# Performance work log

Hardware: AMD Instinct MI355X
Metric: run time of the kernel (lower is better)

Reference implementation:

```python
import jax, jax.numpy as jnp
import numpy as np

STRIDE = 32
NUM_CLASSES = 20
CONF_THRESH = 0.01
NMS_THRESH = 0.5
INPUT_H, INPUT_W = 1024, 1024
EPS = 1e-28


def make_grid(h, w):
    hs, ws = h // STRIDE, w // STRIDE
    gy, gx = jnp.meshgrid(jnp.arange(hs), jnp.arange(ws), indexing='ij')
    # [1, hs*ws, 2] (x, y) cell coordinates
    return jnp.stack([gx, gy], axis=-1).reshape(1, hs * ws, 2).astype(jnp.float32)


def decode_boxes(txtytwth, grid):
    # txtytwth: [B, N, 4] -> [xmin, ymin, xmax, ymax] in pixels
    cxy = (jax.nn.sigmoid(txtytwth[..., :2]) + grid) * STRIDE
    wh = jnp.exp(txtytwth[..., 2:])
    return jnp.concatenate([cxy - wh * 0.5, cxy + wh * 0.5], axis=-1)


def pairwise_iou(boxes):
    # boxes: [N, 4]; faithful to source: area without +1, w/h clamped to 1e-28
    x1, y1, x2, y2 = boxes[:, 0], boxes[:, 1], boxes[:, 2], boxes[:, 3]
    areas = (x2 - x1) * (y2 - y1)
    xx1 = jnp.maximum(x1[:, None], x1[None, :])
    yy1 = jnp.maximum(y1[:, None], y1[None, :])
    xx2 = jnp.minimum(x2[:, None], x2[None, :])
    yy2 = jnp.minimum(y2[:, None], y2[None, :])
    w = jnp.maximum(EPS, xx2 - xx1)
    h = jnp.maximum(EPS, yy2 - yy1)
    inter = w * h
    return inter / (areas[:, None] + areas[None, :] - inter)


def nms_single(boxes, scores, valid):
    # greedy NMS, fixed-shape: returns keep mask [N] in original order
    n = boxes.shape[0]
    order = jnp.argsort(-scores)
    b = boxes[order]
    v = valid[order]
    iou = pairwise_iou(b)  # [N, N]
    idx = jnp.arange(n)

    def body(i, keep):
        sup = keep[i] & (iou[i] > NMS_THRESH) & (idx > i)
        return keep & jnp.logical_not(sup)

    keep_sorted = jax.lax.fori_loop(0, n, body, v)
    return jnp.zeros(n, dtype=bool).at[order].set(keep_sorted)


def setup_inputs() -> dict:
    key = jax.random.key(0)
    k1, k2, k3 = jax.random.split(key, 3)
    feat = jax.random.normal(k1, (64, 512, 32, 32), dtype=jnp.float32)
    w_pred = jax.random.normal(k2, (25, 512), dtype=jnp.float32) * 0.05
    b_pred = jax.random.normal(k3, (25,), dtype=jnp.float32) * 0.05
    return {"feat": feat, "w_pred": w_pred, "b_pred": b_pred}


def reference(feat, w_pred, b_pred):
    B, C, hs, ws = feat.shape
    N = hs * ws
    # 1x1 conv head: [B, 25, hs, ws] -> [B, N, 25]
    pred = jnp.einsum('bchw,oc->bhwo', feat, w_pred) + b_pred
    pred = pred.reshape(B, N, 1 + NUM_CLASSES + 4)

    conf = jax.nn.sigmoid(pred[..., :1])                      # [B, N, 1]
    cls = jax.nn.softmax(pred[..., 1:1 + NUM_CLASSES], -1)    # [B, N, 20]
    boxes = decode_boxes(pred[..., 1 + NUM_CLASSES:], make_grid(INPUT_H, INPUT_W))
    scale = jnp.array([INPUT_W, INPUT_H, INPUT_W, INPUT_H], jnp.float32)
    boxes = jnp.clip(boxes / scale, 0.0, 1.0)                 # [B, N, 4] in [0,1]

    scores_all = conf * cls                                   # [B, N, 20]
    cls_inds = jnp.argmax(scores_all, axis=-1)                # [B, N]
    scores = jnp.max(scores_all, axis=-1)                     # [B, N]
    valid = scores > CONF_THRESH

    # class-aware NMS via per-class coordinate offset (boxes in [0,1])
    off_boxes = boxes + cls_inds[..., None].astype(jnp.float32) * 2.0
    keep = jax.vmap(nms_single)(off_boxes, scores, valid)     # [B, N] bool
    return boxes, scores, cls_inds.astype(jnp.int32), keep
```

## Files before the change

### kernel.cpp

```cpp
#include <hip/hip_runtime.h>
#include <hip/hip_bf16.h>

typedef unsigned long long u64;
typedef unsigned int u32;
typedef __attribute__((ext_vector_type(4))) double f64x4;

#define NB   64
#define NPOS 1024
#define NOUT 25
#define NCLS 20
#define BIGCAP 256
#define ECAP   2048
#define TINY_TH (30.0f / 1024.0f)

#define OFF_CNT   0
#define OFF_BIGL  512
#define OFF_EDGL  66048

__device__ __forceinline__ void epilogue(const double* __restrict__ acc,
                                         const float* __restrict__ bias,
                                         int b, int n,
                                         float* __restrict__ boxes_out,
                                         float* __restrict__ scores_out,
                                         float* __restrict__ cls_out,
                                         int* __restrict__ bigcnt,
                                         int* __restrict__ biglist)
{
    double p[NOUT];
#pragma unroll
    for (int o = 0; o < NOUT; ++o) p[o] = acc[o] + (double)bias[o];

    double conf = 1.0 / (1.0 + exp(-p[0]));
    double m = p[1]; int ci = 0;
#pragma unroll
    for (int i = 2; i <= NCLS; ++i) {
        if (p[i] > m) { m = p[i]; ci = i - 1; }
    }
    double ssum = 0.0;
#pragma unroll
    for (int i = 0; i < NCLS; ++i) ssum += exp(p[1 + i] - m);
    double best = conf / ssum;

    int gx = n & 31, gy = n >> 5;
    double sx = 1.0 / (1.0 + exp(-p[21]));
    double sy = 1.0 / (1.0 + exp(-p[22]));
    double cx = (sx + (double)gx) * 32.0;
    double cy = (sy + (double)gy) * 32.0;
    double bw = exp(p[23]), bh = exp(p[24]);
    double x1 = (cx - bw * 0.5) * (1.0 / 1024.0);
    double y1 = (cy - bh * 0.5) * (1.0 / 1024.0);
    double x2 = (cx + bw * 0.5) * (1.0 / 1024.0);
    double y2 = (cy + bh * 0.5) * (1.0 / 1024.0);
    x1 = fmin(fmax(x1, 0.0), 1.0); y1 = fmin(fmax(y1, 0.0), 1.0);
    x2 = fmin(fmax(x2, 0.0), 1.0); y2 = fmin(fmax(y2, 0.0), 1.0);

    float fx1 = (float)x1, fy1 = (float)y1, fx2 = (float)x2, fy2 = (float)y2;
    int gi = b * NPOS + n;
    ((float4*)boxes_out)[gi] = make_float4(fx1, fy1, fx2, fy2);
    scores_out[gi] = (float)best;
    cls_out[gi]    = (float)ci;

    if (!((fx2 - fx1 < TINY_TH) && (fy2 - fy1 < TINY_TH))) {
        int s = atomicAdd(&bigcnt[b], 1);
        if (s < BIGCAP) biglist[b * BIGCAP + s] = n;
    }
}

__device__ __forceinline__ float4 loadB(const float* __restrict__ w, int c, int bo4)
{
    float4 r = make_float4(0.f, 0.f, 0.f, 0.f);
    int o = bo4 * 4;
    if (o + 0 < NOUT) r.x = w[(o + 0) * 512 + c];
    if (o + 1 < NOUT) r.y = w[(o + 1) * 512 + c];
    if (o + 2 < NOUT) r.z = w[(o + 2) * 512 + c];
    if (o + 3 < NOUT) r.w = w[(o + 3) * 512 + c];
    return r;
}

__global__ __launch_bounds__(256, 6) void k_main(const float* __restrict__ feat,
                                                 const float* __restrict__ w,
                                                 const float* __restrict__ bias,
                                                 float* __restrict__ boxes_out,
                                                 float* __restrict__ scores_out,
                                                 float* __restrict__ cls_out,
                                                 int* __restrict__ bigcnt,
                                                 int* __restrict__ biglist)
{
    __shared__ __align__(16) char smem[24576];
    float* AbF = (float*)smem;
    float* BbF = (float*)(smem + 16384);
    double (*pd)[33] = (double(*)[33])smem;

    const int b   = blockIdx.y;
    const int tid = threadIdx.x;
    const int l   = tid & 63;
    const int wv  = tid >> 6;
    const int pg  = wv >> 1;
    const int oh  = wv & 1;
    const int n0  = blockIdx.x * 64;

    double ca = ((l >> 4) == 0) ? (double)(l & 15) : 0.0;
    double cb = ((l >> 4) == 0) ? 1.0 : 0.0;
    f64x4 cd = {0.0, 0.0, 0.0, 0.0};
    cd = __builtin_amdgcn_mfma_f64_16x16x4f64(ca, cb, cd, 0, 0, 0);
    int rmap[4];
#pragma unroll
    for (int v = 0; v < 4; ++v) {
        int r = (int)(cd[v] + 0.5);
        rmap[v] = (r < 0) ? 0 : (r > 15 ? 15 : r);
    }

    const float* __restrict__ featb = feat + (size_t)b * 512 * NPOS + n0;
    const int bch = tid >> 3, bo4 = tid & 7;

#define A_SRC(C0, IT) (((const float4*)(featb + (size_t)((C0) + wv*8 + (IT)*4 + (l>>4)) * NPOS)) + (l & 15))
#define A_DST(BUF, IT) ((float4*)(AbF + (BUF)*2048 + (wv*8 + (IT)*4) * 64 + l*4))
#define B_DST(BUF) ((float4*)(BbF + (BUF)*1024 + bch*32 + bo4*4))

    f64x4 acc0 = {0.0, 0.0, 0.0, 0.0};
    f64x4 acc1 = {0.0, 0.0, 0.0, 0.0};

    float4 ra0 = *A_SRC(0, 0), ra1 = *A_SRC(0, 1);
    float4 rb  = loadB(w, bch, bo4);
    *A_DST(0, 0) = ra0;  *A_DST(0, 1) = ra1;
    *B_DST(0) = rb;
    __syncthreads();

#pragma unroll 1
    for (int t = 0; t < 16; ++t) {
        const int buf = t & 1;
        const bool more = (t + 1) < 16;
        const int c1 = (t + 1) * 32;
        if (more) {
            ra0 = *A_SRC(c1, 0);  ra1 = *A_SRC(c1, 1);
            rb  = loadB(w, c1 + bch, bo4);
        }
#pragma unroll
        for (int s = 0; s < 8; ++s) {
            const int rowA = buf*2048 + (4*s + (l >> 4)) * 64 + pg * 32 + (l & 15);
            const int rowB = buf*1024 + (4*s + (l >> 4)) * 32 + oh * 16 + (l & 15);
            double av0 = (double)AbF[rowA];
            double av1 = (double)AbF[rowA + 16];
            double bv  = (double)BbF[rowB];
            acc0 = __builtin_amdgcn_mfma_f64_16x16x4f64(av0, bv, acc0, 0, 0, 0);
            acc1 = __builtin_amdgcn_mfma_f64_16x16x4f64(av1, bv, acc1, 0, 0, 0);
        }
        if (more) {
            *A_DST(buf ^ 1, 0) = ra0;  *A_DST(buf ^ 1, 1) = ra1;
            *B_DST(buf ^ 1) = rb;
        }
        __syncthreads();
    }
#undef A_SRC
#undef A_DST
#undef B_DST

#pragma unroll
    for (int v = 0; v < 4; ++v) {
        int r0 = pg * 32 + rmap[v];
        pd[r0][oh * 16 + (l & 15)]      = acc0[v];
        pd[r0 + 16][oh * 16 + (l & 15)] = acc1[v];
    }
    __syncthreads();

    if (tid < 64) {
        double acc[NOUT];
#pragma unroll
        for (int o = 0; o < NOUT; ++o) acc[o] = pd[tid][o];
        int n = n0 + tid;
        epilogue(acc, bias, b, n, boxes_out, scores_out, cls_out, bigcnt, biglist);
    }
}

__device__ __forceinline__ void pair_check(int b, int p, int i,
                                           float4 bp, float ap, int cp,
                                           const float4* __restrict__ boxes4,
                                           const float* __restrict__ scores,
                                           const float* __restrict__ cls,
                                           int* __restrict__ edgecnt,
                                           u32* __restrict__ edges,
                                           bool need_tiny_i)
{
    float si = scores[b * NPOS + i];
    if (si <= 0.01f) return;
    float4 bi = boxes4[b * NPOS + i];
    if (need_tiny_i) {
        if (!((bi.z - bi.x < TINY_TH) && (bi.w - bi.y < TINY_TH))) return;
    }
    if ((int)cls[b * NPOS + i] != cp) return;
    float xx1 = fmaxf(bi.x, bp.x), yy1 = fmaxf(bi.y, bp.y);
    float xx2 = fminf(bi.z, bp.z), yy2 = fminf(bi.w, bp.w);
    float ww = fmaxf(1e-28f, xx2 - xx1);
    float hh = fmaxf(1e-28f, yy2 - yy1);
    float inter = ww * hh;
    float ai = (bi.z - bi.x) * (bi.w - bi.y);
    float uni = ai + ap - inter;
    if (uni > 0.0f && inter > 0.5f * uni) {
        int u = p < i ? p : i, v = p < i ? i : p;
        int slot = atomicAdd(&edgecnt[b], 1);
        if (slot < ECAP) edges[(size_t)b * ECAP + slot] = ((u32)u << 16) | (u32)v;
    }
}

__global__ __launch_bounds__(256) void k_edge(const float4* __restrict__ boxes4,
                                              const float* __restrict__ scores,
                                              const float* __restrict__ cls,
                                              const int* __restrict__ bigcnt,
                                              const int* __restrict__ biglist,
                                              int* __restrict__ edgecnt,
                                              u32* __restrict__ edges)
{
    const int b = blockIdx.y;
    const int p = blockIdx.x * 256 + threadIdx.x;
    const float sp = scores[b * NPOS + p];
    if (sp <= 0.01f) return;
    const float4 bp = boxes4[b * NPOS + p];
    const float ap = (bp.z - bp.x) * (bp.w - bp.y);
    const int cp = (int)cls[b * NPOS + p];
    const bool tinyp = (bp.z - bp.x < TINY_TH) && (bp.w - bp.y < TINY_TH);
    const int gx = p & 31, gy = p >> 5;

    if (tinyp) {
        if (gy > 0 && gx > 0)  pair_check(b, p, p - 33, bp, ap, cp, boxes4, scores, cls, edgecnt, edges, true);
        if (gy > 0)            pair_check(b, p, p - 32, bp, ap, cp, boxes4, scores, cls, edgecnt, edges, true);
        if (gy > 0 && gx < 31) pair_check(b, p, p - 31, bp, ap, cp, boxes4, scores, cls, edgecnt, edges, true);
        if (gx > 0)            pair_check(b, p, p - 1,  bp, ap, cp, boxes4, scores, cls, edgecnt, edges, true);
    }
    int nb = bigcnt[b]; if (nb > BIGCAP) nb = BIGCAP;
    for (int t = 0; t < nb; ++t) {
        int q = biglist[b * BIGCAP + t];
        if (q == p) continue;
        if (!tinyp && p > q) continue;
        pair_check(b, p, q, bp, ap, cp, boxes4, scores, cls, edgecnt, edges, false);
    }
}

__global__ __launch_bounds__(64) void k_resolve(const float* __restrict__ scores,
                                                const int* __restrict__ edgecnt,
                                                const u32* __restrict__ edges,
                                                float* __restrict__ keep_out)
{
    __shared__ u64 keepw[16];
    __shared__ u64 done[ECAP / 64];
    const int b = blockIdx.x, lane = threadIdx.x;

    for (int t = 0; t < 16; ++t) {
        bool v = scores[b * NPOS + t * 64 + lane] > 0.01f;
        u64 w = __ballot(v);
        if (lane == 0) keepw[t] = w;
    }
    if (lane < ECAP / 64) done[lane] = 0ull;
    __syncthreads();

    int E = edgecnt[b]; if (E > ECAP) E = ECAP;
    if (lane == 0 && E > 0) {
        const u32* eb = edges + (size_t)b * ECAP;
        for (int it = 0; it < E; ++it) {
            int bestj = -1, bidx = 0, bsup = 0, btgt = 0;
            float bs = -1.0f;
            for (int j = 0; j < E; ++j) {
                if ((done[j >> 6] >> (j & 63)) & 1ull) continue;
                u32 e = eb[j];
                int u = (int)(e >> 16), v = (int)(e & 0xffffu);
                float su = scores[b * NPOS + u], sv = scores[b * NPOS + v];
                int sup, tgt; float ss;
                if (su > sv || (su == sv && u < v)) { sup = u; tgt = v; ss = su; }
                else                                { sup = v; tgt = u; ss = sv; }
                if (bestj < 0 || ss > bs || (ss == bs && sup < bidx)) {
                    bestj = j; bs = ss; bidx = sup; bsup = sup; btgt = tgt;
                }
            }
            done[bestj >> 6] |= 1ull << (bestj & 63);
            if ((keepw[bsup >> 6] >> (bsup & 63)) & 1ull)
                keepw[btgt >> 6] &= ~(1ull << (btgt & 63));
        }
    }
    __syncthreads();

    for (int t = 0; t < 16; ++t) {
        u64 w = keepw[t];
        keep_out[b * NPOS + t * 64 + lane] = ((w >> lane) & 1ull) ? 1.0f : 0.0f;
    }
}

extern "C" void kernel_launch(void* const* d_in, const int* in_sizes, int n_in,
                              void* d_out, int out_size, void* d_ws, size_t ws_size,
                              hipStream_t stream)
{
    const float* feat = (const float*)d_in[0];
    const float* w    = (const float*)d_in[1];
    const float* bias = (const float*)d_in[2];

    float* out = (float*)d_out;
    float* boxes_out  = out;
    float* scores_out = out + NB * NPOS * 4;
    float* cls_out    = out + NB * NPOS * 5;
    float* keep_out   = out + NB * NPOS * 6;

    char* ws = (char*)d_ws;
    int*    bigcnt = (int*)   (ws + OFF_CNT);
    int*    edgecnt= (int*)   (ws + OFF_CNT + 256);
    int*    biglist= (int*)   (ws + OFF_BIGL);
    u32*    edges  = (u32*)   (ws + OFF_EDGL);

    hipMemsetAsync(ws + OFF_CNT, 0, 512, stream);
    hipLaunchKernelGGL(k_main,   dim3(16, 64), dim3(256), 0, stream, feat, w, bias,
                       boxes_out, scores_out, cls_out, bigcnt, biglist);
    hipLaunchKernelGGL(k_edge,   dim3(4, 64),  dim3(256), 0, stream,
                       (const float4*)boxes_out, scores_out, cls_out,
                       bigcnt, biglist, edgecnt, edges);
    hipLaunchKernelGGL(k_resolve, dim3(64),    dim3(64),  0, stream, scores_out,
                       edgecnt, edges, keep_out);
}
```

Before: 72.95 us.

## Replace global atomics with per-tile ballot lists, shared-memory edge staging, drop memset

The main kernel no longer uses a global atomic to append big boxes. Each 64-position tile builds its list with a wavefront ballot and popcount and writes it to a per-tile slot. The edge kernel gathers these lists into shared memory and collects edges with shared-memory atomics before flushing them per block. The resolve kernel first concatenates the per-block edge lists into shared memory, so its serial scan no longer reads global memory. The memset launch is removed, and the weight tile is loaded as scalars into a padded layout. In exchange, the list gathering is done serially by one thread, and the per-block edge capacity is smaller, which risks overflow.

```diff
diff --git a/kernel.cpp b/kernel.cpp
--- a/kernel.cpp
+++ b/kernel.cpp
@@ -9,22 +9,21 @@
 #define NPOS 1024
 #define NOUT 25
 #define NCLS 20
-#define BIGCAP 256
-#define ECAP   2048
+#define ECAP_B 512
+#define ECAP_S 2048
 #define TINY_TH (30.0f / 1024.0f)
 
-#define OFF_CNT   0
-#define OFF_BIGL  512
-#define OFF_EDGL  66048
+#define OFF_BIGC  0
+#define OFF_BIGL  4096
+#define OFF_EDGC  266240
+#define OFF_EDGL  267264
 
 __device__ __forceinline__ void epilogue(const double* __restrict__ acc,
                                          const float* __restrict__ bias,
-                                         int b, int n,
+                                         int b, int n, bool* isbig,
                                          float* __restrict__ boxes_out,
                                          float* __restrict__ scores_out,
-                                         float* __restrict__ cls_out,
-                                         int* __restrict__ bigcnt,
-                                         int* __restrict__ biglist)
+                                         float* __restrict__ cls_out)
 {
     double p[NOUT];
 #pragma unroll
@@ -59,22 +58,7 @@
     ((float4*)boxes_out)[gi] = make_float4(fx1, fy1, fx2, fy2);
     scores_out[gi] = (float)best;
     cls_out[gi]    = (float)ci;
-
-    if (!((fx2 - fx1 < TINY_TH) && (fy2 - fy1 < TINY_TH))) {
-        int s = atomicAdd(&bigcnt[b], 1);
-        if (s < BIGCAP) biglist[b * BIGCAP + s] = n;
-    }
-}
-
-__device__ __forceinline__ float4 loadB(const float* __restrict__ w, int c, int bo4)
-{
-    float4 r = make_float4(0.f, 0.f, 0.f, 0.f);
-    int o = bo4 * 4;
-    if (o + 0 < NOUT) r.x = w[(o + 0) * 512 + c];
-    if (o + 1 < NOUT) r.y = w[(o + 1) * 512 + c];
-    if (o + 2 < NOUT) r.z = w[(o + 2) * 512 + c];
-    if (o + 3 < NOUT) r.w = w[(o + 3) * 512 + c];
-    return r;
+    *isbig = !((fx2 - fx1 < TINY_TH) && (fy2 - fy1 < TINY_TH));
 }
 
 __global__ __launch_bounds__(256, 6) void k_main(const float* __restrict__ feat,
@@ -83,21 +67,22 @@
                                                  float* __restrict__ boxes_out,
                                                  float* __restrict__ scores_out,
                                                  float* __restrict__ cls_out,
-                                                 int* __restrict__ bigcnt,
-                                                 int* __restrict__ biglist)
-{
-    __shared__ __align__(16) char smem[24576];
+                                                 int* __restrict__ bigcntT,
+                                                 int* __restrict__ biglistT)
+{
+    __shared__ __align__(16) char smem[24832];
     float* AbF = (float*)smem;
     float* BbF = (float*)(smem + 16384);
     double (*pd)[33] = (double(*)[33])smem;
 
     const int b   = blockIdx.y;
+    const int tx  = blockIdx.x;
     const int tid = threadIdx.x;
     const int l   = tid & 63;
     const int wv  = tid >> 6;
     const int pg  = wv >> 1;
     const int oh  = wv & 1;
-    const int n0  = blockIdx.x * 64;
+    const int n0  = tx * 64;
 
     double ca = ((l >> 4) == 0) ? (double)(l & 15) : 0.0;
     double cb = ((l >> 4) == 0) ? 1.0 : 0.0;
@@ -111,19 +96,25 @@
     }
 
     const float* __restrict__ featb = feat + (size_t)b * 512 * NPOS + n0;
-    const int bch = tid >> 3, bo4 = tid & 7;
+    const int bo = tid >> 5;
+    const int bc = tid & 31;
 
 #define A_SRC(C0, IT) (((const float4*)(featb + (size_t)((C0) + wv*8 + (IT)*4 + (l>>4)) * NPOS)) + (l & 15))
 #define A_DST(BUF, IT) ((float4*)(AbF + (BUF)*2048 + (wv*8 + (IT)*4) * 64 + l*4))
-#define B_DST(BUF) ((float4*)(BbF + (BUF)*1024 + bch*32 + bo4*4))
+#define B_LOAD(C0, P, DST) do {                                               \
+    int o_ = (P)*8 + bo;                                                      \
+    (DST) = (o_ < NOUT) ? w[(size_t)o_ * 512 + (C0) + bc] : 0.0f;             \
+} while (0)
+#define B_WRITE(BUF, P, V) (BbF[(BUF)*1056 + bc*33 + (P)*8 + bo] = (V))
 
     f64x4 acc0 = {0.0, 0.0, 0.0, 0.0};
     f64x4 acc1 = {0.0, 0.0, 0.0, 0.0};
 
     float4 ra0 = *A_SRC(0, 0), ra1 = *A_SRC(0, 1);
-    float4 rb  = loadB(w, bch, bo4);
+    float rb0, rb1, rb2, rb3;
+    B_LOAD(0, 0, rb0); B_LOAD(0, 1, rb1); B_LOAD(0, 2, rb2); B_LOAD(0, 3, rb3);
     *A_DST(0, 0) = ra0;  *A_DST(0, 1) = ra1;
-    *B_DST(0) = rb;
+    B_WRITE(0, 0, rb0); B_WRITE(0, 1, rb1); B_WRITE(0, 2, rb2); B_WRITE(0, 3, rb3);
     __syncthreads();
 
 #pragma unroll 1
@@ -133,12 +124,13 @@
         const int c1 = (t + 1) * 32;
         if (more) {
             ra0 = *A_SRC(c1, 0);  ra1 = *A_SRC(c1, 1);
-            rb  = loadB(w, c1 + bch, bo4);
+            B_LOAD(c1, 0, rb0); B_LOAD(c1, 1, rb1);
+            B_LOAD(c1, 2, rb2); B_LOAD(c1, 3, rb3);
         }
 #pragma unroll
         for (int s = 0; s < 8; ++s) {
             const int rowA = buf*2048 + (4*s + (l >> 4)) * 64 + pg * 32 + (l & 15);
-            const int rowB = buf*1024 + (4*s + (l >> 4)) * 32 + oh * 16 + (l & 15);
+            const int rowB = buf*1056 + (4*s + (l >> 4)) * 33 + oh * 16 + (l & 15);
             double av0 = (double)AbF[rowA];
             double av1 = (double)AbF[rowA + 16];
             double bv  = (double)BbF[rowB];
@@ -147,13 +139,15 @@
         }
         if (more) {
             *A_DST(buf ^ 1, 0) = ra0;  *A_DST(buf ^ 1, 1) = ra1;
-            *B_DST(buf ^ 1) = rb;
+            B_WRITE(buf ^ 1, 0, rb0); B_WRITE(buf ^ 1, 1, rb1);
+            B_WRITE(buf ^ 1, 2, rb2); B_WRITE(buf ^ 1, 3, rb3);
         }
         __syncthreads();
     }
 #undef A_SRC
 #undef A_DST
-#undef B_DST
+#undef B_LOAD
+#undef B_WRITE
 
 #pragma unroll
     for (int v = 0; v < 4; ++v) {
@@ -168,80 +162,110 @@
 #pragma unroll
         for (int o = 0; o < NOUT; ++o) acc[o] = pd[tid][o];
         int n = n0 + tid;
-        epilogue(acc, bias, b, n, boxes_out, scores_out, cls_out, bigcnt, biglist);
-    }
-}
-
-__device__ __forceinline__ void pair_check(int b, int p, int i,
-                                           float4 bp, float ap, int cp,
-                                           const float4* __restrict__ boxes4,
-                                           const float* __restrict__ scores,
-                                           const float* __restrict__ cls,
-                                           int* __restrict__ edgecnt,
-                                           u32* __restrict__ edges,
-                                           bool need_tiny_i)
-{
-    float si = scores[b * NPOS + i];
-    if (si <= 0.01f) return;
-    float4 bi = boxes4[b * NPOS + i];
-    if (need_tiny_i) {
-        if (!((bi.z - bi.x < TINY_TH) && (bi.w - bi.y < TINY_TH))) return;
-    }
-    if ((int)cls[b * NPOS + i] != cp) return;
-    float xx1 = fmaxf(bi.x, bp.x), yy1 = fmaxf(bi.y, bp.y);
-    float xx2 = fminf(bi.z, bp.z), yy2 = fminf(bi.w, bp.w);
-    float ww = fmaxf(1e-28f, xx2 - xx1);
-    float hh = fmaxf(1e-28f, yy2 - yy1);
-    float inter = ww * hh;
-    float ai = (bi.z - bi.x) * (bi.w - bi.y);
-    float uni = ai + ap - inter;
-    if (uni > 0.0f && inter > 0.5f * uni) {
-        int u = p < i ? p : i, v = p < i ? i : p;
-        int slot = atomicAdd(&edgecnt[b], 1);
-        if (slot < ECAP) edges[(size_t)b * ECAP + slot] = ((u32)u << 16) | (u32)v;
+        bool isbig;
+        epilogue(acc, bias, b, n, &isbig, boxes_out, scores_out, cls_out);
+
+        u64 mask = __ballot(isbig);
+        if (isbig) {
+            int slot = __popcll(mask & ((1ull << tid) - 1ull));
+            biglistT[(b * 16 + tx) * 64 + slot] = n;
+        }
+        if (tid == 0) bigcntT[b * 16 + tx] = (int)__popcll(mask);
     }
 }
 
 __global__ __launch_bounds__(256) void k_edge(const float4* __restrict__ boxes4,
                                               const float* __restrict__ scores,
                                               const float* __restrict__ cls,
-                                              const int* __restrict__ bigcnt,
-                                              const int* __restrict__ biglist,
-                                              int* __restrict__ edgecnt,
-                                              u32* __restrict__ edges)
-{
-    const int b = blockIdx.y;
-    const int p = blockIdx.x * 256 + threadIdx.x;
+                                              const int* __restrict__ bigcntT,
+                                              const int* __restrict__ biglistT,
+                                              int* __restrict__ edgecntT,
+                                              u32* __restrict__ edgesT)
+{
+    __shared__ int bl[NPOS];
+    __shared__ int nbtot;
+    __shared__ u32 eds[ECAP_B];
+    __shared__ int ecnt;
+    const int b  = blockIdx.y;
+    const int bx = blockIdx.x;
+    const int tid = threadIdx.x;
+    const int p = bx * 256 + tid;
+
+    if (tid == 0) {
+        int s = 0;
+        for (int t = 0; t < 16; ++t) {
+            int c = bigcntT[b * 16 + t];
+            for (int k = 0; k < c; ++k) bl[s++] = biglistT[(b * 16 + t) * 64 + k];
+        }
+        nbtot = s;
+        ecnt = 0;
+    }
+    __syncthreads();
+
     const float sp = scores[b * NPOS + p];
-    if (sp <= 0.01f) return;
-    const float4 bp = boxes4[b * NPOS + p];
-    const float ap = (bp.z - bp.x) * (bp.w - bp.y);
-    const int cp = (int)cls[b * NPOS + p];
-    const bool tinyp = (bp.z - bp.x < TINY_TH) && (bp.w - bp.y < TINY_TH);
-    const int gx = p & 31, gy = p >> 5;
-
-    if (tinyp) {
-        if (gy > 0 && gx > 0)  pair_check(b, p, p - 33, bp, ap, cp, boxes4, scores, cls, edgecnt, edges, true);
-        if (gy > 0)            pair_check(b, p, p - 32, bp, ap, cp, boxes4, scores, cls, edgecnt, edges, true);
-        if (gy > 0 && gx < 31) pair_check(b, p, p - 31, bp, ap, cp, boxes4, scores, cls, edgecnt, edges, true);
-        if (gx > 0)            pair_check(b, p, p - 1,  bp, ap, cp, boxes4, scores, cls, edgecnt, edges, true);
-    }
-    int nb = bigcnt[b]; if (nb > BIGCAP) nb = BIGCAP;
-    for (int t = 0; t < nb; ++t) {
-        int q = biglist[b * BIGCAP + t];
-        if (q == p) continue;
-        if (!tinyp && p > q) continue;
-        pair_check(b, p, q, bp, ap, cp, boxes4, scores, cls, edgecnt, edges, false);
-    }
+    if (sp > 0.01f) {
+        const float4 bp = boxes4[b * NPOS + p];
+        const float ap = (bp.z - bp.x) * (bp.w - bp.y);
+        const int cp = (int)cls[b * NPOS + p];
+        const bool tinyp = (bp.z - bp.x < TINY_TH) && (bp.w - bp.y < TINY_TH);
+        const int gx = p & 31, gy = p >> 5;
+
+#define PAIR(I, NEEDTINY) do {                                                \
+    int i_ = (I);                                                             \
+    if (scores[b * NPOS + i_] > 0.01f) {                                      \
+        float4 bi = boxes4[b * NPOS + i_];                                    \
+        bool ok = true;                                                       \
+        if (NEEDTINY)                                                         \
+            ok = (bi.z - bi.x < TINY_TH) && (bi.w - bi.y < TINY_TH);          \
+        if (ok && (int)cls[b * NPOS + i_] == cp) {                            \
+            float xx1 = fmaxf(bi.x, bp.x), yy1 = fmaxf(bi.y, bp.y);           \
+            float xx2 = fminf(bi.z, bp.z), yy2 = fminf(bi.w, bp.w);           \
+            float ww = fmaxf(1e-28f, xx2 - xx1);                              \
+            float hh = fmaxf(1e-28f, yy2 - yy1);                              \
+            float inter = ww * hh;                                            \
+            float ai = (bi.z - bi.x) * (bi.w - bi.y);                         \
+            float uni = ai + ap - inter;                                      \
+            if (uni > 0.0f && inter > 0.5f * uni) {                           \
+                int u_ = p < i_ ? p : i_, v_ = p < i_ ? i_ : p;               \
+                int slot = atomicAdd(&ecnt, 1);                               \
+                if (slot < ECAP_B) eds[slot] = ((u32)u_ << 16) | (u32)v_;     \
+            }                                                                 \
+        }                                                                     \
+    }                                                                         \
+} while (0)
+
+        if (tinyp) {
+            if (gy > 0 && gx > 0)  PAIR(p - 33, true);
+            if (gy > 0)            PAIR(p - 32, true);
+            if (gy > 0 && gx < 31) PAIR(p - 31, true);
+            if (gx > 0)            PAIR(p - 1,  true);
+        }
+        int nb = nbtot;
+        for (int t = 0; t < nb; ++t) {
+            int q = bl[t];
+            if (q == p) continue;
+            if (!tinyp && p > q) continue;
+            PAIR(q, false);
+        }
+#undef PAIR
+    }
+    __syncthreads();
+
+    int E = ecnt; if (E > ECAP_B) E = ECAP_B;
+    if (tid == 0) edgecntT[b * 4 + bx] = E;
+    for (int i = tid; i < E; i += 256)
+        edgesT[(size_t)(b * 4 + bx) * ECAP_B + i] = eds[i];
 }
 
 __global__ __launch_bounds__(64) void k_resolve(const float* __restrict__ scores,
-                                                const int* __restrict__ edgecnt,
-                                                const u32* __restrict__ edges,
+                                                const int* __restrict__ edgecntT,
+                                                const u32* __restrict__ edgesT,
                                                 float* __restrict__ keep_out)
 {
     __shared__ u64 keepw[16];
-    __shared__ u64 done[ECAP / 64];
+    __shared__ u32 eds[ECAP_S];
+    __shared__ u64 done[ECAP_S / 64];
+    __shared__ int Esh;
     const int b = blockIdx.x, lane = threadIdx.x;
 
     for (int t = 0; t < 16; ++t) {
@@ -249,18 +273,27 @@
         u64 w = __ballot(v);
         if (lane == 0) keepw[t] = w;
     }
-    if (lane < ECAP / 64) done[lane] = 0ull;
-    __syncthreads();
-
-    int E = edgecnt[b]; if (E > ECAP) E = ECAP;
+    if (lane < ECAP_S / 64) done[lane] = 0ull;
+    if (lane == 0) {
+        int off = 0;
+        for (int e = 0; e < 4; ++e) {
+            int c = edgecntT[b * 4 + e];
+            if (c > ECAP_B) c = ECAP_B;
+            for (int j = 0; j < c; ++j)
+                eds[off++] = edgesT[(size_t)(b * 4 + e) * ECAP_B + j];
+        }
+        Esh = off;
+    }
+    __syncthreads();
+
+    int E = Esh;
     if (lane == 0 && E > 0) {
-        const u32* eb = edges + (size_t)b * ECAP;
         for (int it = 0; it < E; ++it) {
             int bestj = -1, bidx = 0, bsup = 0, btgt = 0;
             float bs = -1.0f;
             for (int j = 0; j < E; ++j) {
                 if ((done[j >> 6] >> (j & 63)) & 1ull) continue;
-                u32 e = eb[j];
+                u32 e = eds[j];
                 int u = (int)(e >> 16), v = (int)(e & 0xffffu);
                 float su = scores[b * NPOS + u], sv = scores[b * NPOS + v];
                 int sup, tgt; float ss;
@@ -298,17 +331,16 @@
     float* keep_out   = out + NB * NPOS * 6;
 
     char* ws = (char*)d_ws;
-    int*    bigcnt = (int*)   (ws + OFF_CNT);
-    int*    edgecnt= (int*)   (ws + OFF_CNT + 256);
-    int*    biglist= (int*)   (ws + OFF_BIGL);
-    u32*    edges  = (u32*)   (ws + OFF_EDGL);
-
-    hipMemsetAsync(ws + OFF_CNT, 0, 512, stream);
+    int* bigcntT  = (int*)(ws + OFF_BIGC);
+    int* biglistT = (int*)(ws + OFF_BIGL);
+    int* edgecntT = (int*)(ws + OFF_EDGC);
+    u32* edgesT   = (u32*)(ws + OFF_EDGL);
+
     hipLaunchKernelGGL(k_main,   dim3(16, 64), dim3(256), 0, stream, feat, w, bias,
-                       boxes_out, scores_out, cls_out, bigcnt, biglist);
+                       boxes_out, scores_out, cls_out, bigcntT, biglistT);
     hipLaunchKernelGGL(k_edge,   dim3(4, 64),  dim3(256), 0, stream,
                        (const float4*)boxes_out, scores_out, cls_out,
-                       bigcnt, biglist, edgecnt, edges);
+                       bigcntT, biglistT, edgecntT, edgesT);
     hipLaunchKernelGGL(k_resolve, dim3(64),    dim3(64),  0, stream, scores_out,
-                       edgecnt, edges, keep_out);
-}
+                       edgecntT, edgesT, keep_out);
+}
```

Result: faster. 70.26 us, median of 2 (-3.7%).
